# Optimization experiments

Measured on AMD Instinct MI355X. Metric: run time of the kernel, lower is better.

Reference implementation:

```python
import jax, jax.numpy as jnp
import numpy as np

D = 1024      # in_features
H = 4096      # hidden_dims
E = 8         # expert_nums
K = 2         # top_k
B, S = 4, 2048


def setup_inputs() -> dict:
    key = jax.random.key(0)
    ks = jax.random.split(key, 8)
    def lin(k, fan_in, shape):
        bound = 1.0 / np.sqrt(fan_in)
        return jax.random.uniform(k, shape, jnp.float32, -bound, bound)
    return {
        "x":  jax.random.normal(ks[0], (B, S, D), jnp.float32),
        "Wg": lin(ks[1], D, (D, E)),
        "bg": lin(ks[2], D, (E,)),
        "W1": lin(ks[3], D, (E, D, H)),
        "b1": lin(ks[4], D, (E, H)),
        "W2": lin(ks[5], H, (E, H, D)),
        "b2": lin(ks[6], H, (E, D)),
    }


def reference(x, Wg, bg, W1, b1, W2, b2):
    B_, S_, D_ = x.shape
    xt = x.reshape(-1, D_)                                   # [N, D]
    # Router: softmax gating + top-k
    logits = xt @ Wg + bg                                    # [N, E]
    scores = jax.nn.softmax(logits, axis=-1)
    topk_probs, topk_idx = jax.lax.top_k(scores, K)          # [N, K]
    # Dense per-expert FFN (the source runs every expert on all tokens)
    h = jnp.einsum("nd,edh->enh", xt, W1) + b1[:, None, :]   # [E, N, H]
    h = jax.nn.gelu(h, approximate=False)
    eo = jnp.einsum("enh,ehd->end", h, W2) + b2[:, None, :]  # [E, N, D]
    # Gather selected experts per token and combine with gate weights
    eo = jnp.transpose(eo, (1, 0, 2))                        # [N, E, D]
    sel = jnp.take_along_axis(eo, topk_idx[:, :, None], axis=1)  # [N, K, D]
    out = jnp.einsum("nk,nkd->nd", topk_probs, sel)          # [N, D]
    return out.reshape(B_, S_, D_)
```

## Files before the change

kernel.cpp:

```cpp
#include <hip/hip_runtime.h>
#include <hip/hip_bf16.h>
#include <cstdint>
#include <cstddef>

using bf16 = __hip_bfloat16;
using short8 = __attribute__((ext_vector_type(8))) short;
using floatx4 = __attribute__((ext_vector_type(4))) float;

constexpr int D_IN = 1024;
constexpr int H_DIM = 4096;
constexpr int E_NUM = 8;
constexpr int NTOK = 8192;
constexpr int NPAIR = NTOK * 2;
constexpr int MAXTILES = 144;

constexpr size_t OFF_PTOK  = 1024;
constexpr size_t OFF_PPROB = 263168;
constexpr size_t OFF_SCHED = 525312;
constexpr size_t OFF_XBF   = 1048576;
constexpr size_t OFF_W2T   = OFF_XBF + (size_t)NTOK * D_IN * 2;
constexpr size_t OFF_HBUF  = OFF_W2T + (size_t)E_NUM * D_IN * H_DIM * 2;
constexpr size_t OFF_W1T   = OFF_HBUF + (size_t)NPAIR * H_DIM * 2;

__device__ __forceinline__ void cp16(const bf16* g, bf16* s) {
  __builtin_amdgcn_global_load_lds(
      (const __attribute__((address_space(1))) unsigned int*)g,
      (__attribute__((address_space(3))) unsigned int*)s, 16, 0, 0);
}

__global__ __launch_bounds__(256) void transpose_cvt(
    const float* __restrict__ in, bf16* __restrict__ out, int K, int N) {
  __shared__ float tile[32][33];
  const int e = blockIdx.z;
  const float* ip = in + (size_t)e * K * N + (size_t)(blockIdx.y * 32) * N + blockIdx.x * 32;
  bf16* op = out + (size_t)e * K * N + (size_t)(blockIdx.x * 32) * K + blockIdx.y * 32;
  const int tx = threadIdx.x & 31, ty = threadIdx.x >> 5;
#pragma unroll
  for (int r = 0; r < 4; r++)
    tile[ty + r * 8][tx] = ip[(size_t)(ty + r * 8) * N + tx];
  __syncthreads();
#pragma unroll
  for (int r = 0; r < 4; r++)
    op[(size_t)(ty + r * 8) * K + tx] = __float2bfloat16(tile[tx][ty + r * 8]);
}

__global__ __launch_bounds__(256) void router_kernel(
    const float* __restrict__ x, const float* __restrict__ Wg,
    const float* __restrict__ bg, bf16* __restrict__ Xbf,
    int* __restrict__ counts, int* __restrict__ pairTok, float* __restrict__ pairProb) {
  const int lane = threadIdx.x & 63;
  const int n = blockIdx.x * 4 + (threadIdx.x >> 6);
  const float* xr = x + (size_t)n * D_IN;
  bf16* xbr = Xbf + (size_t)n * D_IN;
  float logit[E_NUM];
#pragma unroll
  for (int e = 0; e < E_NUM; e++) logit[e] = 0.f;
#pragma unroll
  for (int i = 0; i < 16; i++) {
    const int d = i * 64 + lane;
    const float xd = xr[d];
    xbr[d] = __float2bfloat16(xd);
    const float4* wr = (const float4*)(Wg + (size_t)d * E_NUM);
    const float4 w0 = wr[0], w1 = wr[1];
    logit[0] += xd * w0.x; logit[1] += xd * w0.y;
    logit[2] += xd * w0.z; logit[3] += xd * w0.w;
    logit[4] += xd * w1.x; logit[5] += xd * w1.y;
    logit[6] += xd * w1.z; logit[7] += xd * w1.w;
  }
#pragma unroll
  for (int e = 0; e < E_NUM; e++) {
#pragma unroll
    for (int off = 32; off >= 1; off >>= 1)
      logit[e] += __shfl_xor(logit[e], off, 64);
  }
  if (lane == 0) {
    float l[E_NUM], mx = -1e30f;
#pragma unroll
    for (int e = 0; e < E_NUM; e++) { l[e] = logit[e] + bg[e]; mx = fmaxf(mx, l[e]); }
    float ex[E_NUM], s = 0.f;
#pragma unroll
    for (int e = 0; e < E_NUM; e++) { ex[e] = expf(l[e] - mx); s += ex[e]; }
    int i0 = 0;
#pragma unroll
    for (int e = 1; e < E_NUM; e++) if (l[e] > l[i0]) i0 = e;
    int i1 = (i0 == 0) ? 1 : 0;
#pragma unroll
    for (int e = 0; e < E_NUM; e++) if (e != i0 && l[e] > l[i1]) i1 = e;
    const float inv = 1.f / s;
    int pos = atomicAdd(&counts[i0], 1);
    pairTok[i0 * NTOK + pos] = n;
    pairProb[i0 * NTOK + pos] = ex[i0] * inv;
    pos = atomicAdd(&counts[i1], 1);
    pairTok[i1 * NTOK + pos] = n | (1 << 15);
    pairProb[i1 * NTOK + pos] = ex[i1] * inv;
  }
}

__global__ void sched_kernel(const int* __restrict__ counts, int* __restrict__ sched) {
  if (threadIdx.x == 0 && blockIdx.x == 0) {
    int* bases = sched;
    int* nTiles = sched + 8;
    int* tileMap = sched + 16;
    int base = 0, t = 0;
    for (int e = 0; e < E_NUM; e++) {
      bases[e] = base;
      const int nt = (counts[e] + 127) >> 7;
      for (int m = 0; m < nt; m++) tileMap[t++] = (e << 16) | m;
      base += counts[e];
    }
    *nTiles = t;
  }
}

template <int MODE, int K, int NC, int NTX>
__global__ __launch_bounds__(256) void gemm_kernel(
    const bf16* __restrict__ A, const bf16* __restrict__ Wt,
    const float* __restrict__ bias, const int* __restrict__ counts,
    const int* __restrict__ pairTok, const float* __restrict__ pairProb,
    const int* __restrict__ sched, bf16* __restrict__ Hout, float* __restrict__ Out) {
  const int nblk = blockIdx.x % NTX;
  const int tix = blockIdx.x / NTX;
  if (tix >= sched[8]) return;
  const int packed = sched[16 + tix];
  const int e = packed >> 16;
  const int m0 = (packed & 0xFFFF) * 128;
  const int cnt = counts[e];
  const int base = sched[e];
  const int n0 = nblk * 128;

  __shared__ __align__(16) bf16 As[128 * 32];
  __shared__ __align__(16) bf16 Bs[128 * 32];

  const int t = threadIdx.x;
  const int lane = t & 63;
  const int wave = t >> 6;
  const int wmq = wave >> 1, wnq = wave & 1;
  const int fr = lane & 15;
  const int kg = (lane >> 4) * 8;

  const bf16* aSrc[2];
  const bf16* bSrc[2];
#pragma unroll
  for (int i = 0; i < 2; i++) {
    const int lin = i * 256 + t;
    const int r = lin >> 2;
    const int c8 = (lin & 3) * 8;
    int p = m0 + r;
    if (p > cnt - 1) p = cnt - 1;
    if (MODE == 0) {
      const int tok = pairTok[e * NTOK + p] & 0x1FFF;
      aSrc[i] = A + (size_t)tok * K + c8;
    } else {
      aSrc[i] = A + (size_t)(base + p) * K + c8;
    }
    bSrc[i] = Wt + ((size_t)e * NC + n0 + r) * K + c8;
  }

  floatx4 acc[4][4];
#pragma unroll
  for (int ti = 0; ti < 4; ti++)
#pragma unroll
    for (int tj = 0; tj < 4; tj++)
      acc[ti][tj] = {0.f, 0.f, 0.f, 0.f};

  for (int k0 = 0; k0 < K; k0 += 32) {
#pragma unroll
    for (int i = 0; i < 2; i++) {
      cp16(aSrc[i] + k0, &As[(size_t)(i * 256 + t) * 8]);
      cp16(bSrc[i] + k0, &Bs[(size_t)(i * 256 + t) * 8]);
    }
    __syncthreads();
    short8 a[4], b[4];
#pragma unroll
    for (int ti = 0; ti < 4; ti++)
      a[ti] = *(const short8*)&As[(wmq * 64 + ti * 16 + fr) * 32 + kg];
#pragma unroll
    for (int tj = 0; tj < 4; tj++)
      b[tj] = *(const short8*)&Bs[(wnq * 64 + tj * 16 + fr) * 32 + kg];
#pragma unroll
    for (int ti = 0; ti < 4; ti++)
#pragma unroll
      for (int tj = 0; tj < 4; tj++)
        acc[ti][tj] = __builtin_amdgcn_mfma_f32_16x16x32_bf16(a[ti], b[tj], acc[ti][tj], 0, 0, 0);
    __syncthreads();
  }

  float bv[4];
#pragma unroll
  for (int tj = 0; tj < 4; tj++)
    bv[tj] = bias[(size_t)e * NC + n0 + wnq * 64 + tj * 16 + fr];

#pragma unroll
  for (int ti = 0; ti < 4; ti++) {
    const int rb = wmq * 64 + ti * 16 + (lane >> 4) * 4;
#pragma unroll
    for (int i = 0; i < 4; i++) {
      const int p = m0 + rb + i;
      if (p < cnt) {
        if (MODE == 0) {
          bf16* orow = Hout + (size_t)(base + p) * NC + n0 + wnq * 64 + fr;
#pragma unroll
          for (int tj = 0; tj < 4; tj++) {
            const float h = acc[ti][tj][i] + bv[tj];
            const float g = 0.5f * h * (1.f + erff(h * 0.70710678118f));
            orow[tj * 16] = __float2bfloat16(g);
          }
        } else {
          const int pt = pairTok[e * NTOK + p];
          const float pr = pairProb[e * NTOK + p];
          const int tok = pt & 0x1FFF;
          float* orow = Out + (size_t)tok * NC + n0 + wnq * 64 + fr;
#pragma unroll
          for (int tj = 0; tj < 4; tj++)
            atomicAdd(&orow[tj * 16], (acc[ti][tj][i] + bv[tj]) * pr);
        }
      }
    }
  }
}

extern "C" void kernel_launch(void* const* d_in, const int* in_sizes, int n_in,
                              void* d_out, int out_size, void* d_ws, size_t ws_size,
                              hipStream_t stream) {
  const float* x  = (const float*)d_in[0];
  const float* Wg = (const float*)d_in[1];
  const float* bg = (const float*)d_in[2];
  const float* W1 = (const float*)d_in[3];
  const float* b1 = (const float*)d_in[4];
  const float* W2 = (const float*)d_in[5];
  const float* b2 = (const float*)d_in[6];
  float* out = (float*)d_out;
  char* ws = (char*)d_ws;

  int*   counts   = (int*)ws;
  int*   pairTok  = (int*)(ws + OFF_PTOK);
  float* pairProb = (float*)(ws + OFF_PPROB);
  int*   sched    = (int*)(ws + OFF_SCHED);
  bf16*  Xbf      = (bf16*)(ws + OFF_XBF);
  bf16*  W2t      = (bf16*)(ws + OFF_W2T);
  bf16*  Hbuf     = (bf16*)(ws + OFF_HBUF);
  bf16*  W1t      = (bf16*)(ws + OFF_W1T);

  hipMemsetAsync(counts, 0, 64, stream);
  hipMemsetAsync(out, 0, (size_t)out_size * sizeof(float), stream);
  transpose_cvt<<<dim3(H_DIM / 32, D_IN / 32, E_NUM), 256, 0, stream>>>(W1, W1t, D_IN, H_DIM);
  transpose_cvt<<<dim3(D_IN / 32, H_DIM / 32, E_NUM), 256, 0, stream>>>(W2, W2t, H_DIM, D_IN);
  router_kernel<<<NTOK / 4, 256, 0, stream>>>(x, Wg, bg, Xbf, counts, pairTok, pairProb);
  sched_kernel<<<1, 64, 0, stream>>>(counts, sched);
  gemm_kernel<0, D_IN, H_DIM, 32><<<32 * MAXTILES, 256, 0, stream>>>(
      Xbf, W1t, b1, counts, pairTok, pairProb, sched, Hbuf, out);
  gemm_kernel<1, H_DIM, D_IN, 8><<<8 * MAXTILES, 256, 0, stream>>>(
      Hbuf, W2t, b2, counts, pairTok, pairProb, sched, Hbuf, out);
}
```

Before: 1.013 ms.

## Double-buffer GEMM loads, vectorize transpose, replace atomics with slot buffer plus combine

```diff
diff --git a/kernel.cpp b/kernel.cpp
--- a/kernel.cpp
+++ b/kernel.cpp
@@ -22,26 +22,28 @@
 constexpr size_t OFF_HBUF  = OFF_W2T + (size_t)E_NUM * D_IN * H_DIM * 2;
 constexpr size_t OFF_W1T   = OFF_HBUF + (size_t)NPAIR * H_DIM * 2;
 
-__device__ __forceinline__ void cp16(const bf16* g, bf16* s) {
-  __builtin_amdgcn_global_load_lds(
-      (const __attribute__((address_space(1))) unsigned int*)g,
-      (__attribute__((address_space(3))) unsigned int*)s, 16, 0, 0);
-}
-
 __global__ __launch_bounds__(256) void transpose_cvt(
     const float* __restrict__ in, bf16* __restrict__ out, int K, int N) {
-  __shared__ float tile[32][33];
+  __shared__ float tile[64][65];
   const int e = blockIdx.z;
-  const float* ip = in + (size_t)e * K * N + (size_t)(blockIdx.y * 32) * N + blockIdx.x * 32;
-  bf16* op = out + (size_t)e * K * N + (size_t)(blockIdx.x * 32) * K + blockIdx.y * 32;
-  const int tx = threadIdx.x & 31, ty = threadIdx.x >> 5;
-#pragma unroll
-  for (int r = 0; r < 4; r++)
-    tile[ty + r * 8][tx] = ip[(size_t)(ty + r * 8) * N + tx];
+  const float* ip = in + (size_t)e * K * N + (size_t)(blockIdx.y * 64) * N + blockIdx.x * 64;
+  bf16* op = out + (size_t)e * K * N + (size_t)(blockIdx.x * 64) * K + blockIdx.y * 64;
+  const int tc = threadIdx.x & 15;
+  const int tr = threadIdx.x >> 4;
+#pragma unroll
+  for (int r = 0; r < 4; r++) {
+    const float4 v = *(const float4*)&ip[(size_t)(tr + r * 16) * N + tc * 4];
+    *(float4*)&tile[tr + r * 16][tc * 4] = v;
+  }
   __syncthreads();
 #pragma unroll
-  for (int r = 0; r < 4; r++)
-    op[(size_t)(ty + r * 8) * K + tx] = __float2bfloat16(tile[tx][ty + r * 8]);
+  for (int r = 0; r < 4; r++) {
+    const int n = tr + r * 16;
+    union { ushort4 u4; bf16 h[4]; } uu;
+#pragma unroll
+    for (int j = 0; j < 4; j++) uu.h[j] = __float2bfloat16(tile[tc * 4 + j][n]);
+    *(ushort4*)&op[(size_t)n * K + tc * 4] = uu.u4;
+  }
 }
 
 __global__ __launch_bounds__(256) void router_kernel(
@@ -117,7 +119,7 @@
     const bf16* __restrict__ A, const bf16* __restrict__ Wt,
     const float* __restrict__ bias, const int* __restrict__ counts,
     const int* __restrict__ pairTok, const float* __restrict__ pairProb,
-    const int* __restrict__ sched, bf16* __restrict__ Hout, float* __restrict__ Out) {
+    const int* __restrict__ sched, bf16* __restrict__ Hout, float* __restrict__ Rout) {
   const int nblk = blockIdx.x % NTX;
   const int tix = blockIdx.x / NTX;
   if (tix >= sched[8]) return;
@@ -128,8 +130,8 @@
   const int base = sched[e];
   const int n0 = nblk * 128;
 
-  __shared__ __align__(16) bf16 As[128 * 32];
-  __shared__ __align__(16) bf16 Bs[128 * 32];
+  __shared__ __align__(16) bf16 As[2][128 * 32];
+  __shared__ __align__(16) bf16 Bs[2][128 * 32];
 
   const int t = threadIdx.x;
   const int lane = t & 63;
@@ -140,11 +142,13 @@
 
   const bf16* aSrc[2];
   const bf16* bSrc[2];
+  int dstOff[2];
 #pragma unroll
   for (int i = 0; i < 2; i++) {
     const int lin = i * 256 + t;
     const int r = lin >> 2;
     const int c8 = (lin & 3) * 8;
+    dstOff[i] = lin * 8;
     int p = m0 + r;
     if (p > cnt - 1) p = cnt - 1;
     if (MODE == 0) {
@@ -156,6 +160,19 @@
     bSrc[i] = Wt + ((size_t)e * NC + n0 + r) * K + c8;
   }
 
+  short8 ra[2], rb[2];
+#pragma unroll
+  for (int i = 0; i < 2; i++) {
+    ra[i] = *(const short8*)aSrc[i];
+    rb[i] = *(const short8*)bSrc[i];
+  }
+#pragma unroll
+  for (int i = 0; i < 2; i++) {
+    *(short8*)&As[0][dstOff[i]] = ra[i];
+    *(short8*)&Bs[0][dstOff[i]] = rb[i];
+  }
+  __syncthreads();
+
   floatx4 acc[4][4];
 #pragma unroll
   for (int ti = 0; ti < 4; ti++)
@@ -163,26 +180,50 @@
     for (int tj = 0; tj < 4; tj++)
       acc[ti][tj] = {0.f, 0.f, 0.f, 0.f};
 
-  for (int k0 = 0; k0 < K; k0 += 32) {
+  constexpr int NIT = K / 32;
+#pragma unroll 2
+  for (int it = 0; it < NIT - 1; ++it) {
+    const int cur = it & 1;
+    const int nxt = cur ^ 1;
+    const int k0 = (it + 1) * 32;
 #pragma unroll
     for (int i = 0; i < 2; i++) {
-      cp16(aSrc[i] + k0, &As[(size_t)(i * 256 + t) * 8]);
-      cp16(bSrc[i] + k0, &Bs[(size_t)(i * 256 + t) * 8]);
-    }
-    __syncthreads();
+      ra[i] = *(const short8*)(aSrc[i] + k0);
+      rb[i] = *(const short8*)(bSrc[i] + k0);
+    }
     short8 a[4], b[4];
 #pragma unroll
     for (int ti = 0; ti < 4; ti++)
-      a[ti] = *(const short8*)&As[(wmq * 64 + ti * 16 + fr) * 32 + kg];
+      a[ti] = *(const short8*)&As[cur][(wmq * 64 + ti * 16 + fr) * 32 + kg];
 #pragma unroll
     for (int tj = 0; tj < 4; tj++)
-      b[tj] = *(const short8*)&Bs[(wnq * 64 + tj * 16 + fr) * 32 + kg];
+      b[tj] = *(const short8*)&Bs[cur][(wnq * 64 + tj * 16 + fr) * 32 + kg];
 #pragma unroll
     for (int ti = 0; ti < 4; ti++)
 #pragma unroll
       for (int tj = 0; tj < 4; tj++)
         acc[ti][tj] = __builtin_amdgcn_mfma_f32_16x16x32_bf16(a[ti], b[tj], acc[ti][tj], 0, 0, 0);
+#pragma unroll
+    for (int i = 0; i < 2; i++) {
+      *(short8*)&As[nxt][dstOff[i]] = ra[i];
+      *(short8*)&Bs[nxt][dstOff[i]] = rb[i];
+    }
     __syncthreads();
+  }
+  {
+    const int cur = (NIT - 1) & 1;
+    short8 a[4], b[4];
+#pragma unroll
+    for (int ti = 0; ti < 4; ti++)
+      a[ti] = *(const short8*)&As[cur][(wmq * 64 + ti * 16 + fr) * 32 + kg];
+#pragma unroll
+    for (int tj = 0; tj < 4; tj++)
+      b[tj] = *(const short8*)&Bs[cur][(wnq * 64 + tj * 16 + fr) * 32 + kg];
+#pragma unroll
+    for (int ti = 0; ti < 4; ti++)
+#pragma unroll
+      for (int tj = 0; tj < 4; tj++)
+        acc[ti][tj] = __builtin_amdgcn_mfma_f32_16x16x32_bf16(a[ti], b[tj], acc[ti][tj], 0, 0, 0);
   }
 
   float bv[4];
@@ -192,10 +233,10 @@
 
 #pragma unroll
   for (int ti = 0; ti < 4; ti++) {
-    const int rb = wmq * 64 + ti * 16 + (lane >> 4) * 4;
+    const int rb2 = wmq * 64 + ti * 16 + (lane >> 4) * 4;
 #pragma unroll
     for (int i = 0; i < 4; i++) {
-      const int p = m0 + rb + i;
+      const int p = m0 + rb2 + i;
       if (p < cnt) {
         if (MODE == 0) {
           bf16* orow = Hout + (size_t)(base + p) * NC + n0 + wnq * 64 + fr;
@@ -208,15 +249,24 @@
         } else {
           const int pt = pairTok[e * NTOK + p];
           const float pr = pairProb[e * NTOK + p];
-          const int tok = pt & 0x1FFF;
-          float* orow = Out + (size_t)tok * NC + n0 + wnq * 64 + fr;
+          const int tok = pt & 0x1FFF, slot = (pt >> 15) & 1;
+          float* orow = Rout + ((size_t)(tok * 2 + slot)) * NC + n0 + wnq * 64 + fr;
 #pragma unroll
           for (int tj = 0; tj < 4; tj++)
-            atomicAdd(&orow[tj * 16], (acc[ti][tj][i] + bv[tj]) * pr);
+            orow[tj * 16] = (acc[ti][tj][i] + bv[tj]) * pr;
         }
       }
     }
   }
+}
+
+__global__ __launch_bounds__(256) void combine_kernel(
+    const float4* __restrict__ r, float4* __restrict__ o) {
+  const int j = blockIdx.x * 256 + threadIdx.x;
+  const int n = j >> 8, c = j & 255;
+  const float4 a = r[(size_t)(n * 2) * 256 + c];
+  const float4 b = r[(size_t)(n * 2 + 1) * 256 + c];
+  o[j] = make_float4(a.x + b.x, a.y + b.y, a.z + b.z, a.w + b.w);
 }
 
 extern "C" void kernel_launch(void* const* d_in, const int* in_sizes, int n_in,
@@ -240,15 +290,16 @@
   bf16*  W2t      = (bf16*)(ws + OFF_W2T);
   bf16*  Hbuf     = (bf16*)(ws + OFF_HBUF);
   bf16*  W1t      = (bf16*)(ws + OFF_W1T);
+  float* resbuf   = (float*)W1t;
 
   hipMemsetAsync(counts, 0, 64, stream);
-  hipMemsetAsync(out, 0, (size_t)out_size * sizeof(float), stream);
-  transpose_cvt<<<dim3(H_DIM / 32, D_IN / 32, E_NUM), 256, 0, stream>>>(W1, W1t, D_IN, H_DIM);
-  transpose_cvt<<<dim3(D_IN / 32, H_DIM / 32, E_NUM), 256, 0, stream>>>(W2, W2t, H_DIM, D_IN);
+  transpose_cvt<<<dim3(H_DIM / 64, D_IN / 64, E_NUM), 256, 0, stream>>>(W1, W1t, D_IN, H_DIM);
+  transpose_cvt<<<dim3(D_IN / 64, H_DIM / 64, E_NUM), 256, 0, stream>>>(W2, W2t, H_DIM, D_IN);
   router_kernel<<<NTOK / 4, 256, 0, stream>>>(x, Wg, bg, Xbf, counts, pairTok, pairProb);
   sched_kernel<<<1, 64, 0, stream>>>(counts, sched);
   gemm_kernel<0, D_IN, H_DIM, 32><<<32 * MAXTILES, 256, 0, stream>>>(
-      Xbf, W1t, b1, counts, pairTok, pairProb, sched, Hbuf, out);
+      Xbf, W1t, b1, counts, pairTok, pairProb, sched, Hbuf, resbuf);
   gemm_kernel<1, H_DIM, D_IN, 8><<<8 * MAXTILES, 256, 0, stream>>>(
-      Hbuf, W2t, b2, counts, pairTok, pairProb, sched, Hbuf, out);
-}
+      Hbuf, W2t, b2, counts, pairTok, pairProb, sched, Hbuf, resbuf);
+  combine_kernel<<<(NTOK * D_IN / 4) / 256, 256, 0, stream>>>((const float4*)resbuf, (float4*)out);
+}
```

Measured after the change: 987.9 us. -2.4%, faster.
